# Kernel tuning notes

Hardware: AMD Instinct MI355X
Metric: run time of the kernel (lower is better)

## Reference

```python
import jax, jax.numpy as jnp
import numpy as np

N_NODES = 4_000_000
N_GRAPHS = 4096  # B; fixed for jit (torch derives it from batch.max()+1)
D_FEAT = 8
NUM_CLASSES = 10


def setup_inputs() -> dict:
    key = jax.random.key(0)
    k1, k2, k3, k4, k5 = jax.random.split(key, 5)
    x = jax.random.normal(k1, (N_NODES, D_FEAT), dtype=jnp.float32)
    # sorted segment ids; with ~977 nodes/graph expected, empty segments are vanishingly unlikely
    batch_ids = jnp.sort(jax.random.randint(k2, (N_NODES,), 0, N_GRAPHS, dtype=jnp.int64))
    input_ids = jax.random.randint(k3, (N_GRAPHS, 128), 0, 30522, dtype=jnp.int64)
    attention_mask = jnp.ones((N_GRAPHS, 128), dtype=jnp.int64)
    W = jax.random.normal(k4, (NUM_CLASSES, D_FEAT), dtype=jnp.float32) * (1.0 / np.sqrt(D_FEAT))
    b = jax.random.normal(k5, (NUM_CLASSES,), dtype=jnp.float32) * 0.01
    return {"x": x, "batch_ids": batch_ids, "input_ids": input_ids,
            "attention_mask": attention_mask, "W": W, "b": b}


def reference(x, batch_ids, input_ids, attention_mask, W, b):
    # Segment-mean pooling: replaces the O(B) python loop of masked means
    # with a single-pass scatter-add. input_ids / attention_mask are unused
    # by the original forward (kept for signature fidelity).
    sums = jax.ops.segment_sum(x, batch_ids, num_segments=N_GRAPHS)          # [B, 8]
    counts = jax.ops.segment_sum(jnp.ones((x.shape[0],), x.dtype), batch_ids,
                                 num_segments=N_GRAPHS)                      # [B]
    pooled = sums / counts[:, None]                                          # [B, 8]
    logits = pooled @ W.T + b                                                # [B, 10]
    return logits
```

## Files before the change

kernel.cpp:

```cpp
#include <hip/hip_runtime.h>

constexpr int N_NODES  = 4000000;
constexpr int N_GRAPHS = 4096;
constexpr int D_FEAT   = 8;
constexpr int N_CLS    = 10;
constexpr int GPB      = 4;
constexpr int WIN      = 16384;

typedef float f32x4 __attribute__((ext_vector_type(4)));

__global__ __launch_bounds__(256) void fused_pool_linear(
    const float* __restrict__ x,
    const int*   __restrict__ ids,
    const float* __restrict__ W,
    const float* __restrict__ bias,
    float*       __restrict__ out)
{
    const f32x4* xf = (const f32x4*)x;
    int wid  = threadIdx.x >> 6;
    int lane = threadIdx.x & 63;
    int g    = blockIdx.x * GPB + wid;

    int half = lane >> 5;
    int l32  = lane & 31;
    int target = g + half;

    int est = (int)((long long)target * N_NODES / N_GRAPHS);
    int lo = est - WIN; if (lo < 0) lo = 0;
    int hi = est + WIN; if (hi > N_NODES) hi = N_NODES;
    {
        bool okL = (lo == 0)       || (ids[lo - 1] < target);
        bool okR = (hi == N_NODES) || (ids[hi] >= target);
        if (!(okL && okR)) { lo = 0; hi = N_NODES; }
    }

    while (hi - lo > 32) {
        int chunk = (hi - lo + 31) >> 5;
        int pos = lo + l32 * chunk;
        int v = (pos < hi) ? ids[pos] : 0x7fffffff;
        unsigned long long m = __ballot(v < target);
        unsigned int mm = half ? (unsigned int)(m >> 32) : (unsigned int)m;
        int cnt = __popc(mm);
        int nlo = cnt ? lo + (cnt - 1) * chunk + 1 : lo;
        int nhi = (cnt < 32) ? min(lo + cnt * chunk, hi) : hi;
        lo = nlo; hi = nhi;
    }
    {
        int pos = lo + l32;
        int v = (pos < hi) ? ids[pos] : 0x7fffffff;
        unsigned long long m = __ballot(v < target);
        unsigned int mm = half ? (unsigned int)(m >> 32) : (unsigned int)m;
        lo += __popc(mm);
    }
    int s = __shfl(lo, 0);
    int e = __shfl(lo, 32);
    int len  = e - s;
    int endf = 2 * e;

    f32x4 a0 = (f32x4)(0.f), a1 = (f32x4)(0.f),
          a2 = (f32x4)(0.f), a3 = (f32x4)(0.f);
    for (int i = 2 * s + lane; i < endf; i += 256) {
        a0 += xf[i];
        if (i +  64 < endf) a1 += xf[i +  64];
        if (i + 128 < endf) a2 += xf[i + 128];
        if (i + 192 < endf) a3 += xf[i + 192];
    }
    f32x4 acc = (a0 + a1) + (a2 + a3);

    #pragma unroll
    for (int off = 32; off >= 2; off >>= 1) {
        acc.x += __shfl_xor(acc.x, off);
        acc.y += __shfl_xor(acc.y, off);
        acc.z += __shfl_xor(acc.z, off);
        acc.w += __shfl_xor(acc.w, off);
    }
    f32x4 other;
    other.x = __shfl_xor(acc.x, 1);
    other.y = __shfl_xor(acc.y, 1);
    other.z = __shfl_xor(acc.z, 1);
    other.w = __shfl_xor(acc.w, 1);

    __shared__ float red[GPB][D_FEAT];
    __shared__ float linv[GPB];
    if (lane == 0) {
        red[wid][0] = acc.x;   red[wid][1] = acc.y;
        red[wid][2] = acc.z;   red[wid][3] = acc.w;
        red[wid][4] = other.x; red[wid][5] = other.y;
        red[wid][6] = other.z; red[wid][7] = other.w;
        linv[wid]   = 1.0f / (float)len;
    }
    __syncthreads();
    if (threadIdx.x < GPB * N_CLS) {
        int j = threadIdx.x / N_CLS;
        int c = threadIdx.x % N_CLS;
        float inv = linv[j];
        const float* w = W + (size_t)c * D_FEAT;
        float a = bias[c];
        #pragma unroll
        for (int k = 0; k < D_FEAT; ++k)
            a += (red[j][k] * inv) * w[k];
        out[((size_t)blockIdx.x * GPB + j) * N_CLS + c] = a;
    }
}

extern "C" void kernel_launch(void* const* d_in, const int* in_sizes, int n_in,
                              void* d_out, int out_size, void* d_ws, size_t ws_size,
                              hipStream_t stream) {
    const float* x   = (const float*)d_in[0];
    const int*   ids = (const int*)d_in[1];
    const float* W   = (const float*)d_in[4];
    const float* b   = (const float*)d_in[5];
    float*       out = (float*)d_out;

    fused_pool_linear<<<N_GRAPHS / GPB, 256, 0, stream>>>(x, ids, W, b, out);
}
```

Baseline: 29.89 us.

## Split each graph's node range across two waves and unguard the main loop

Each block now handles 2 graphs with 4 waves, so each graph's node range is split in half between two waves. The grid doubles to 2048 blocks, and a launch-bounds occupancy hint is added. The partial sums from the two waves are combined in shared memory before the linear layer. The accumulation loop becomes an unguarded 4-way unrolled body plus a scalar tail, which removes per-load bounds checks. The aim is more memory-level parallelism for this bandwidth-bound pass; the cost is that both waves of a graph repeat the same binary search over the ids.

```diff
diff --git a/kernel.cpp b/kernel.cpp
--- a/kernel.cpp
+++ b/kernel.cpp
@@ -4,12 +4,12 @@
 constexpr int N_GRAPHS = 4096;
 constexpr int D_FEAT   = 8;
 constexpr int N_CLS    = 10;
-constexpr int GPB      = 4;
+constexpr int GPB      = 2;
 constexpr int WIN      = 16384;
 
 typedef float f32x4 __attribute__((ext_vector_type(4)));
 
-__global__ __launch_bounds__(256) void fused_pool_linear(
+__global__ __launch_bounds__(256, 8) void fused_pool_linear(
     const float* __restrict__ x,
     const int*   __restrict__ ids,
     const float* __restrict__ W,
@@ -17,9 +17,11 @@
     float*       __restrict__ out)
 {
     const f32x4* xf = (const f32x4*)x;
-    int wid  = threadIdx.x >> 6;
-    int lane = threadIdx.x & 63;
-    int g    = blockIdx.x * GPB + wid;
+    int wid   = threadIdx.x >> 6;
+    int lane  = threadIdx.x & 63;
+    int gslot = wid >> 1;
+    int part  = wid & 1;
+    int g     = blockIdx.x * GPB + gslot;
 
     int half = lane >> 5;
     int l32  = lane & 31;
@@ -54,17 +56,26 @@
     }
     int s = __shfl(lo, 0);
     int e = __shfl(lo, 32);
-    int len  = e - s;
-    int endf = 2 * e;
+    int len = e - s;
+    int mid = s + (len >> 1);
+    int r0  = part ? mid : s;
+    int r1  = part ? e   : mid;
+
+    int i    = 2 * r0 + lane;
+    int endf = 2 * r1;
+    int nf4  = endf - 2 * r0;
+    int iters = nf4 >> 8;
 
     f32x4 a0 = (f32x4)(0.f), a1 = (f32x4)(0.f),
           a2 = (f32x4)(0.f), a3 = (f32x4)(0.f);
-    for (int i = 2 * s + lane; i < endf; i += 256) {
+    for (int it = 0; it < iters; ++it, i += 256) {
         a0 += xf[i];
-        if (i +  64 < endf) a1 += xf[i +  64];
-        if (i + 128 < endf) a2 += xf[i + 128];
-        if (i + 192 < endf) a3 += xf[i + 192];
+        a1 += xf[i +  64];
+        a2 += xf[i + 128];
+        a3 += xf[i + 192];
     }
+    for (; i < endf; i += 64)
+        a0 += xf[i];
     f32x4 acc = (a0 + a1) + (a2 + a3);
 
     #pragma unroll
@@ -80,14 +91,14 @@
     other.z = __shfl_xor(acc.z, 1);
     other.w = __shfl_xor(acc.w, 1);
 
-    __shared__ float red[GPB][D_FEAT];
+    __shared__ float red[4][D_FEAT];
     __shared__ float linv[GPB];
     if (lane == 0) {
         red[wid][0] = acc.x;   red[wid][1] = acc.y;
         red[wid][2] = acc.z;   red[wid][3] = acc.w;
         red[wid][4] = other.x; red[wid][5] = other.y;
         red[wid][6] = other.z; red[wid][7] = other.w;
-        linv[wid]   = 1.0f / (float)len;
+        if (part == 0) linv[gslot] = 1.0f / (float)len;
     }
     __syncthreads();
     if (threadIdx.x < GPB * N_CLS) {
@@ -98,7 +109,7 @@
         float a = bias[c];
         #pragma unroll
         for (int k = 0; k < D_FEAT; ++k)
-            a += (red[j][k] * inv) * w[k];
+            a += (red[2 * j][k] + red[2 * j + 1][k]) * inv * w[k];
         out[((size_t)blockIdx.x * GPB + j) * N_CLS + c] = a;
     }
 }
```

Result: slower. 31.47 us (+5.3%).

## Find block-level segment bounds once and derive inner boundaries by scanning ids

Applied to the files above, without the earlier changes.

Every wave used to binary-search its own pair of segment boundaries. Now each block binary-searches only the outer boundaries of its four-graph range. The inner boundaries come from a parallel scan of adjacent ids that writes change points into shared memory. The accumulation loop is split into an unguarded unrolled body plus a tail, and the final linear layer is done per wave with shuffles instead of a shared-memory reduction. This cuts the redundant search traffic and the per-iteration bounds checks, but it adds a pass over the block's ids, two extra barriers and a serial fixup for empty segments. The search window is also halved.

```diff
diff --git a/kernel.cpp b/kernel.cpp
--- a/kernel.cpp
+++ b/kernel.cpp
@@ -5,11 +5,11 @@
 constexpr int D_FEAT   = 8;
 constexpr int N_CLS    = 10;
 constexpr int GPB      = 4;
-constexpr int WIN      = 16384;
+constexpr int WIN      = 8192;
 
 typedef float f32x4 __attribute__((ext_vector_type(4)));
 
-__global__ __launch_bounds__(256) void fused_pool_linear(
+__global__ __launch_bounds__(256) void fused_all(
     const float* __restrict__ x,
     const int*   __restrict__ ids,
     const float* __restrict__ W,
@@ -17,13 +17,12 @@
     float*       __restrict__ out)
 {
     const f32x4* xf = (const f32x4*)x;
+    int g0   = blockIdx.x * GPB;
     int wid  = threadIdx.x >> 6;
     int lane = threadIdx.x & 63;
-    int g    = blockIdx.x * GPB + wid;
-
     int half = lane >> 5;
     int l32  = lane & 31;
-    int target = g + half;
+    int target = g0 + half * GPB;
 
     int est = (int)((long long)target * N_NODES / N_GRAPHS);
     int lo = est - WIN; if (lo < 0) lo = 0;
@@ -54,17 +53,39 @@
     }
     int s = __shfl(lo, 0);
     int e = __shfl(lo, 32);
-    int len  = e - s;
-    int endf = 2 * e;
+
+    __shared__ int lb[GPB + 1];
+    if (threadIdx.x < GPB + 1) lb[threadIdx.x] = -1;
+    __syncthreads();
+    if (threadIdx.x == 0) { lb[0] = s; lb[GPB] = e; }
+    for (int i = s + 1 + (int)threadIdx.x; i < e; i += 256) {
+        int cur  = ids[i];
+        int prev = ids[i - 1];
+        if (cur != prev) {
+            for (int k = prev + 1; k <= cur; ++k) lb[k - g0] = i;
+        }
+    }
+    __syncthreads();
+    if (threadIdx.x == 0) {
+        for (int k = GPB - 1; k >= 1; --k) if (lb[k] < 0) lb[k] = lb[k + 1];
+    }
+    __syncthreads();
+
+    int gs = lb[wid];
+    int ge = lb[wid + 1];
 
     f32x4 a0 = (f32x4)(0.f), a1 = (f32x4)(0.f),
           a2 = (f32x4)(0.f), a3 = (f32x4)(0.f);
-    for (int i = 2 * s + lane; i < endf; i += 256) {
+    int i    = 2 * gs + lane;
+    int endf = 2 * ge;
+    int full = (endf - 2 * gs) >> 8;
+    for (int it = 0; it < full; ++it, i += 256) {
         a0 += xf[i];
-        if (i +  64 < endf) a1 += xf[i +  64];
-        if (i + 128 < endf) a2 += xf[i + 128];
-        if (i + 192 < endf) a3 += xf[i + 192];
+        a1 += xf[i +  64];
+        a2 += xf[i + 128];
+        a3 += xf[i + 192];
     }
+    for (; i < endf; i += 64) a0 += xf[i];
     f32x4 acc = (a0 + a1) + (a2 + a3);
 
     #pragma unroll
@@ -74,32 +95,20 @@
         acc.z += __shfl_xor(acc.z, off);
         acc.w += __shfl_xor(acc.w, off);
     }
-    f32x4 other;
-    other.x = __shfl_xor(acc.x, 1);
-    other.y = __shfl_xor(acc.y, 1);
-    other.z = __shfl_xor(acc.z, 1);
-    other.w = __shfl_xor(acc.w, 1);
+    float m0 = __shfl(acc.x, 0), m1 = __shfl(acc.y, 0);
+    float m2 = __shfl(acc.z, 0), m3 = __shfl(acc.w, 0);
+    float m4 = __shfl(acc.x, 1), m5 = __shfl(acc.y, 1);
+    float m6 = __shfl(acc.z, 1), m7 = __shfl(acc.w, 1);
 
-    __shared__ float red[GPB][D_FEAT];
-    __shared__ float linv[GPB];
-    if (lane == 0) {
-        red[wid][0] = acc.x;   red[wid][1] = acc.y;
-        red[wid][2] = acc.z;   red[wid][3] = acc.w;
-        red[wid][4] = other.x; red[wid][5] = other.y;
-        red[wid][6] = other.z; red[wid][7] = other.w;
-        linv[wid]   = 1.0f / (float)len;
-    }
-    __syncthreads();
-    if (threadIdx.x < GPB * N_CLS) {
-        int j = threadIdx.x / N_CLS;
-        int c = threadIdx.x % N_CLS;
-        float inv = linv[j];
-        const float* w = W + (size_t)c * D_FEAT;
-        float a = bias[c];
-        #pragma unroll
-        for (int k = 0; k < D_FEAT; ++k)
-            a += (red[j][k] * inv) * w[k];
-        out[((size_t)blockIdx.x * GPB + j) * N_CLS + c] = a;
+    if (lane < N_CLS) {
+        float inv = 1.0f / (float)(ge - gs);
+        const float* w = W + (size_t)lane * D_FEAT;
+        float a = bias[lane];
+        a += (m0 * inv) * w[0] + (m1 * inv) * w[1]
+           + (m2 * inv) * w[2] + (m3 * inv) * w[3]
+           + (m4 * inv) * w[4] + (m5 * inv) * w[5]
+           + (m6 * inv) * w[6] + (m7 * inv) * w[7];
+        out[(size_t)(g0 + wid) * N_CLS + lane] = a;
     }
 }
 
@@ -112,5 +121,5 @@
     const float* b   = (const float*)d_in[5];
     float*       out = (float*)d_out;
 
-    fused_pool_linear<<<N_GRAPHS / GPB, 256, 0, stream>>>(x, ids, W, b, out);
+    fused_all<<<N_GRAPHS / GPB, 256, 0, stream>>>(x, ids, W, b, out);
 }
```

Measured after the change: 32.52 us. 1.09x slower.
